# Kernel tuning notes

Measured on AMD Instinct MI355X. Metric: run time of the kernel, lower is better.

## Reference

```python
import jax, jax.numpy as jnp
import numpy as np

EMBED_DIM = 512
NUM_HEADS = 8
HEAD_DIM = EMBED_DIM // NUM_HEADS
K_NEIGH = 3
SEQ_N = 16384
BATCH = 4


def setup_inputs() -> dict:
    key = jax.random.key(0)
    ks = jax.random.split(key, 12)
    x = jax.random.normal(ks[0], (BATCH, SEQ_N, EMBED_DIM), dtype=jnp.float32)
    neighbor_table = jax.random.randint(ks[1], (K_NEIGH, SEQ_N), 0, SEQ_N, dtype=jnp.int64)
    s = 0.02
    Wq = jax.random.normal(ks[2], (EMBED_DIM, EMBED_DIM), jnp.float32) * s
    bq = jnp.zeros((EMBED_DIM,), jnp.float32)
    Wk = jax.random.normal(ks[3], (EMBED_DIM, EMBED_DIM), jnp.float32) * s
    bk = jnp.zeros((EMBED_DIM,), jnp.float32)
    Wv = jax.random.normal(ks[4], (EMBED_DIM, EMBED_DIM), jnp.float32) * s
    bv = jnp.zeros((EMBED_DIM,), jnp.float32)
    Wo = jax.random.normal(ks[5], (EMBED_DIM, EMBED_DIM), jnp.float32) * s
    bo = jnp.zeros((EMBED_DIM,), jnp.float32)
    return {"x": x, "neighbor_table": neighbor_table,
            "Wq": Wq, "bq": bq, "Wk": Wk, "bk": bk,
            "Wv": Wv, "bv": bv, "Wo": Wo, "bo": bo}


def reference(x, neighbor_table, Wq, bq, Wk, bk, Wv, bv, Wo, bo):
    B, N, C = x.shape
    H, d = NUM_HEADS, HEAD_DIM
    scale = d ** (-0.5)
    # buffers derived from neighbor_table (matches module __init__)
    valid = (neighbor_table != -1)                      # (K, N)
    idx = jnp.clip(neighbor_table, 0)                   # (K, N)

    # projections; nn.Linear: y = x @ W.T + b
    def proj(W, b):
        return (jnp.einsum('bnc,oc->bno', x, W) + b).reshape(B, N, H, d).transpose(0, 2, 1, 3)  # (B,H,N,d)

    q = proj(Wq, bq)
    k = proj(Wk, bk)
    v = proj(Wv, bv)

    # gather neighbors: (B, H, K, N, d)
    k_nb = k[:, :, idx, :]
    v_nb = v[:, :, idx, :]

    # scores over head_dim: (B, H, K, N)
    scores = jnp.einsum('bhnd,bhknd->bhkn', q, k_nb) * scale
    scores = jnp.where(valid[None, None], scores, -jnp.inf)
    attn = jax.nn.softmax(scores, axis=2)               # softmax over K neighbors
    # dropout is identity (eval / p used only at train)

    out = jnp.einsum('bhkn,bhknd->bhnd', attn, v_nb)    # (B,H,N,d)
    out = out.transpose(0, 2, 1, 3).reshape(B, N, C)
    out = jnp.einsum('bnc,oc->bno', out, Wo) + bo
    return out
```

## Files before the change

### kernel.cpp

```cpp
#include <hip/hip_runtime.h>
#include <stdint.h>

#define SEQN 16384
#define NBATCH 4

typedef __attribute__((ext_vector_type(8))) __bf16 bf16x8;
typedef __attribute__((ext_vector_type(4))) float f32x4;
typedef __attribute__((ext_vector_type(4))) unsigned int u32x4;

__device__ __forceinline__ unsigned int f2bf(float f) {
  unsigned int x = __builtin_bit_cast(unsigned int, f);
  x = x + 0x7fffu + ((x >> 16) & 1u);
  return x >> 16;
}
__device__ __forceinline__ float bf2f(unsigned int lo) {
  return __builtin_bit_cast(float, lo << 16);
}

__device__ __forceinline__ void gload_lds16(const unsigned short* g, unsigned char* l) {
  __builtin_amdgcn_global_load_lds(
      (const __attribute__((address_space(1))) unsigned int*)g,
      (__attribute__((address_space(3))) unsigned int*)l, 16, 0, 0);
}

template<bool OUT_BF16>
__global__ __launch_bounds__(256, 2)
void gemm_bt(const unsigned short* __restrict__ A,
             const unsigned short* __restrict__ Bt,
             const float* __restrict__ bias,
             void* __restrict__ Cout,
             int Ncols, int K)
{
  __shared__ __align__(16) unsigned char lA[128 * 64 * 2];
  __shared__ __align__(16) unsigned char lB[128 * 64 * 2];
  const int tid = threadIdx.x;
  const int lane = tid & 63;
  const int wid = tid >> 6;
  const int wr = (wid >> 1) * 64;
  const int wc = (wid & 1) * 64;
  const int nbx = Ncols >> 7;
  const int bx = (int)blockIdx.x % nbx;
  const int by = (int)blockIdx.x / nbx;
  const long row0 = (long)by << 7;
  const int col0 = bx << 7;

  f32x4 acc[4][4];
#pragma unroll
  for (int i = 0; i < 4; ++i)
#pragma unroll
    for (int j = 0; j < 4; ++j) acc[i][j] = (f32x4)0.0f;

  for (int kt = 0; kt < K; kt += 64) {
#pragma unroll
    for (int i = 0; i < 4; ++i) {
      const int f = i * 256 + tid;
      const int r = f >> 3;
      const int cd = (f & 7) ^ (r & 7);
      gload_lds16(A + (row0 + r) * (long)K + kt + cd * 8, lA + f * 16);
      gload_lds16(Bt + (long)(col0 + r) * K + kt + cd * 8, lB + f * 16);
    }
    __syncthreads();
#pragma unroll
    for (int kk = 0; kk < 2; ++kk) {
      bf16x8 af[4], bfv[4];
#pragma unroll
      for (int fm = 0; fm < 4; ++fm) {
        const int row = wr + fm * 16 + (lane & 15);
        const int ch = (kk * 4 + (lane >> 4)) ^ (row & 7);
        af[fm] = __builtin_bit_cast(bf16x8, *(const u32x4*)(lA + row * 128 + ch * 16));
      }
#pragma unroll
      for (int fn = 0; fn < 4; ++fn) {
        const int row = wc + fn * 16 + (lane & 15);
        const int ch = (kk * 4 + (lane >> 4)) ^ (row & 7);
        bfv[fn] = __builtin_bit_cast(bf16x8, *(const u32x4*)(lB + row * 128 + ch * 16));
      }
#pragma unroll
      for (int fm = 0; fm < 4; ++fm)
#pragma unroll
        for (int fn = 0; fn < 4; ++fn)
          acc[fm][fn] = __builtin_amdgcn_mfma_f32_16x16x32_bf16(af[fm], bfv[fn], acc[fm][fn], 0, 0, 0);
    }
    __syncthreads();
  }

#pragma unroll
  for (int fn = 0; fn < 4; ++fn) {
    const int n = col0 + wc + fn * 16 + (lane & 15);
    const float bn = bias[n];
#pragma unroll
    for (int fm = 0; fm < 4; ++fm) {
      const long mbase = row0 + wr + fm * 16 + ((lane >> 4) << 2);
#pragma unroll
      for (int j = 0; j < 4; ++j) {
        const float v = acc[fm][fn][j] + bn;
        if constexpr (OUT_BF16)
          ((unsigned short*)Cout)[(mbase + j) * (long)Ncols + n] = (unsigned short)f2bf(v);
        else
          ((float*)Cout)[(mbase + j) * (long)Ncols + n] = v;
      }
    }
  }
}

__global__ __launch_bounds__(256)
void nbr_attn(const unsigned short* __restrict__ qkv,
              const int* __restrict__ nbr,
              unsigned short* __restrict__ aout)
{
  const int wid = (int)((blockIdx.x * 256 + threadIdx.x) >> 6);
  const int lane = threadIdx.x & 63;
  const int n = wid & (SEQN - 1);
  const int b = wid >> 14;

  const unsigned short* qrow = qkv + (size_t)wid * 1536;
  float qv[8];
  {
    const u32x4 raw = *(const u32x4*)(qrow + lane * 8);
#pragma unroll
    for (int i = 0; i < 4; ++i) {
      qv[2 * i] = bf2f(raw[i] & 0xffffu);
      qv[2 * i + 1] = bf2f(raw[i] >> 16);
    }
  }
  float s[3];
  u32x4 vraw[3];
  bool val[3];
#pragma unroll
  for (int k = 0; k < 3; ++k) {
    const int t = nbr[k * SEQN + n];
    val[k] = (t != -1);
    const int j = t > 0 ? t : 0;
    const unsigned short* krow = qkv + ((size_t)(b * SEQN + j)) * 1536 + 512;
    const u32x4 kraw = *(const u32x4*)(krow + lane * 8);
    vraw[k] = *(const u32x4*)(krow + 512 + lane * 8);
    float d = 0.f;
#pragma unroll
    for (int i = 0; i < 4; ++i)
      d += qv[2 * i] * bf2f(kraw[i] & 0xffffu) + qv[2 * i + 1] * bf2f(kraw[i] >> 16);
    d += __shfl_xor(d, 1);
    d += __shfl_xor(d, 2);
    d += __shfl_xor(d, 4);
    s[k] = d * 0.125f;
  }
  float m = -3.0e38f;
#pragma unroll
  for (int k = 0; k < 3; ++k)
    if (val[k]) m = fmaxf(m, s[k]);
  float e[3], sum = 0.f;
#pragma unroll
  for (int k = 0; k < 3; ++k) {
    e[k] = val[k] ? __expf(s[k] - m) : 0.f;
    sum += e[k];
  }
  const float inv = sum > 0.f ? 1.f / sum : 0.f;
  float acc[8] = {0.f, 0.f, 0.f, 0.f, 0.f, 0.f, 0.f, 0.f};
#pragma unroll
  for (int k = 0; k < 3; ++k) {
    const float w = e[k] * inv;
#pragma unroll
    for (int i = 0; i < 4; ++i) {
      acc[2 * i] += w * bf2f(vraw[k][i] & 0xffffu);
      acc[2 * i + 1] += w * bf2f(vraw[k][i] >> 16);
    }
  }
  u32x4 o;
#pragma unroll
  for (int i = 0; i < 4; ++i)
    o[i] = f2bf(acc[2 * i]) | (f2bf(acc[2 * i + 1]) << 16);
  *(u32x4*)(aout + (size_t)wid * 512 + lane * 8) = o;
}

__global__ __launch_bounds__(256)
void cvt_f32_bf16(const float* __restrict__ in, unsigned short* __restrict__ out, int n8) {
  int i = blockIdx.x * 256 + threadIdx.x;
  const int stride = gridDim.x * 256;
  for (; i < n8; i += stride) {
    const float4* p = (const float4*)(in + (size_t)i * 8);
    const float4 a = p[0], c = p[1];
    u32x4 o;
    o[0] = f2bf(a.x) | (f2bf(a.y) << 16);
    o[1] = f2bf(a.z) | (f2bf(a.w) << 16);
    o[2] = f2bf(c.x) | (f2bf(c.y) << 16);
    o[3] = f2bf(c.z) | (f2bf(c.w) << 16);
    *(u32x4*)(out + (size_t)i * 8) = o;
  }
}

__global__ __launch_bounds__(256)
void prep_w(const float* __restrict__ Wq, const float* __restrict__ Wk,
            const float* __restrict__ Wv, const float* __restrict__ Wo,
            const float* __restrict__ bq, const float* __restrict__ bk,
            const float* __restrict__ bv,
            unsigned short* __restrict__ wf, unsigned short* __restrict__ wo,
            float* __restrict__ biasf)
{
  const int i = blockIdx.x * 256 + threadIdx.x;
  const int stride = gridDim.x * 256;
  for (int t = i; t < 262144; t += stride) {
    wf[t] = (unsigned short)f2bf(Wq[t]);
    wf[262144 + t] = (unsigned short)f2bf(Wk[t]);
    wf[524288 + t] = (unsigned short)f2bf(Wv[t]);
    wo[t] = (unsigned short)f2bf(Wo[t]);
  }
  if (i < 512) {
    biasf[i] = bq[i];
    biasf[512 + i] = bk[i];
    biasf[1024 + i] = bv[i];
  }
}

extern "C" void kernel_launch(void* const* d_in, const int* in_sizes, int n_in,
                              void* d_out, int out_size, void* d_ws, size_t ws_size,
                              hipStream_t stream) {
  const float* x  = (const float*)d_in[0];
  const int* nbr  = (const int*)d_in[1];
  const float* Wq = (const float*)d_in[2];
  const float* bq = (const float*)d_in[3];
  const float* Wk = (const float*)d_in[4];
  const float* bk = (const float*)d_in[5];
  const float* Wv = (const float*)d_in[6];
  const float* bv = (const float*)d_in[7];
  const float* Wo = (const float*)d_in[8];
  const float* bo = (const float*)d_in[9];
  float* out = (float*)d_out;
  unsigned char* ws = (unsigned char*)d_ws;

  unsigned short* xb  = (unsigned short*)(ws);
  unsigned short* qkv = (unsigned short*)(ws + 67108864UL);
  unsigned short* wf  = (unsigned short*)(ws + 268435456UL);
  unsigned short* wo  = (unsigned short*)(ws + 270008320UL);
  float* biasf        = (float*)(ws + 270532608UL);

  cvt_f32_bf16<<<4096, 256, 0, stream>>>(x, xb, 33554432 / 8);
  prep_w<<<1024, 256, 0, stream>>>(Wq, Wk, Wv, Wo, bq, bk, bv, wf, wo, biasf);
  gemm_bt<true><<<dim3(512 * 12), 256, 0, stream>>>(xb, wf, biasf, qkv, 1536, 512);
  nbr_attn<<<16384, 256, 0, stream>>>(qkv, nbr, xb);
  gemm_bt<false><<<dim3(512 * 4), 256, 0, stream>>>(xb, wo, bo, out, 512, 512);
}
```

Baseline: 298.5 us.

## Rewrite GEMM as 256x256-tile, 4-stage pipelined kernel with XCD-aware block swizzle

Replaces the 128x128 single-buffered GEMM with a 512-thread 256x256-tile kernel that keeps four K-slices of 32 in flight in 128 KB of dynamic LDS, using explicit vmcnt waits so global-to-LDS loads overlap the MFMA work. Block IDs are remapped across the eight XCDs to improve L2 reuse, and MFMA sections raise wave priority. The larger tile reduces global traffic per FLOP, at the cost of one block per CU, a hard-coded K=512, and fewer blocks for the output projection (512 blocks).

```diff
diff --git a/kernel.cpp b/kernel.cpp
--- a/kernel.cpp
+++ b/kernel.cpp
@@ -24,72 +24,112 @@
 }
 
 template<bool OUT_BF16>
-__global__ __launch_bounds__(256, 2)
-void gemm_bt(const unsigned short* __restrict__ A,
+__global__ __launch_bounds__(512, 1)
+void gemm256(const unsigned short* __restrict__ A,
              const unsigned short* __restrict__ Bt,
              const float* __restrict__ bias,
              void* __restrict__ Cout,
-             int Ncols, int K)
+             int Ncols)
 {
-  __shared__ __align__(16) unsigned char lA[128 * 64 * 2];
-  __shared__ __align__(16) unsigned char lB[128 * 64 * 2];
+  extern __shared__ __align__(16) unsigned char smem[];
+  const int K = 512;
   const int tid = threadIdx.x;
   const int lane = tid & 63;
   const int wid = tid >> 6;
-  const int wr = (wid >> 1) * 64;
-  const int wc = (wid & 1) * 64;
-  const int nbx = Ncols >> 7;
-  const int bx = (int)blockIdx.x % nbx;
-  const int by = (int)blockIdx.x / nbx;
-  const long row0 = (long)by << 7;
-  const int col0 = bx << 7;
-
-  f32x4 acc[4][4];
-#pragma unroll
-  for (int i = 0; i < 4; ++i)
+  const int wr = (wid >> 2) << 7;
+  const int wc = (wid & 3) << 6;
+  const int nbx = Ncols >> 8;
+  const int nwg = (int)gridDim.x;
+  const int bid = (int)blockIdx.x;
+  const int cpx = nwg >> 3;
+  const int swz = (bid & 7) * cpx + (bid >> 3);
+  const int bx = swz % nbx;
+  const int by = swz / nbx;
+  const long row0 = (long)by << 8;
+  const int col0 = bx << 8;
+
+  int srcA[2], srcB[2];
+#pragma unroll
+  for (int i = 0; i < 2; ++i) {
+    const int G = i * 512 + tid;
+    const int r = G >> 2;
+    const int c = (G & 3) ^ ((G >> 3) & 3);
+    srcA[i] = (int)(row0 + r) * K + c * 8;
+    srcB[i] = (col0 + r) * K + c * 8;
+  }
+
+  int aoff[8], boff[4];
+#pragma unroll
+  for (int fm = 0; fm < 8; ++fm) {
+    const int r = wr + fm * 16 + (lane & 15);
+    aoff[fm] = r * 64 + ((((lane >> 4)) ^ ((r >> 1) & 3)) << 4);
+  }
+#pragma unroll
+  for (int fn = 0; fn < 4; ++fn) {
+    const int r = wc + fn * 16 + (lane & 15);
+    boff[fn] = r * 64 + ((((lane >> 4)) ^ ((r >> 1) & 3)) << 4);
+  }
+
+  f32x4 acc[8][4];
+#pragma unroll
+  for (int i = 0; i < 8; ++i)
 #pragma unroll
     for (int j = 0; j < 4; ++j) acc[i][j] = (f32x4)0.0f;
 
-  for (int kt = 0; kt < K; kt += 64) {
-#pragma unroll
-    for (int i = 0; i < 4; ++i) {
-      const int f = i * 256 + tid;
-      const int r = f >> 3;
-      const int cd = (f & 7) ^ (r & 7);
-      gload_lds16(A + (row0 + r) * (long)K + kt + cd * 8, lA + f * 16);
-      gload_lds16(Bt + (long)(col0 + r) * K + kt + cd * 8, lB + f * 16);
-    }
+#define STAGE(t)                                                            \
+  {                                                                         \
+    unsigned char* buf_ = smem + ((t) & 3) * 32768;                         \
+    const int kt_ = (t) * 32;                                               \
+    gload_lds16(A + srcA[0] + kt_, buf_ + tid * 16);                        \
+    gload_lds16(Bt + srcB[0] + kt_, buf_ + 16384 + tid * 16);               \
+    gload_lds16(A + srcA[1] + kt_, buf_ + 8192 + tid * 16);                 \
+    gload_lds16(Bt + srcB[1] + kt_, buf_ + 24576 + tid * 16);               \
+  }
+
+#define COMPUTE(t)                                                          \
+  {                                                                         \
+    const unsigned char* buf_ = smem + ((t) & 3) * 32768;                   \
+    bf16x8 af[8], bfv[4];                                                   \
+    _Pragma("unroll")                                                       \
+    for (int fm = 0; fm < 8; ++fm)                                          \
+      af[fm] = __builtin_bit_cast(bf16x8, *(const u32x4*)(buf_ + aoff[fm]));\
+    _Pragma("unroll")                                                       \
+    for (int fn = 0; fn < 4; ++fn)                                          \
+      bfv[fn] = __builtin_bit_cast(bf16x8,                                  \
+                    *(const u32x4*)(buf_ + 16384 + boff[fn]));              \
+    __builtin_amdgcn_s_setprio(1);                                          \
+    _Pragma("unroll")                                                       \
+    for (int fm = 0; fm < 8; ++fm)                                          \
+      _Pragma("unroll")                                                     \
+      for (int fn = 0; fn < 4; ++fn)                                        \
+        acc[fm][fn] = __builtin_amdgcn_mfma_f32_16x16x32_bf16(              \
+            af[fm], bfv[fn], acc[fm][fn], 0, 0, 0);                         \
+    __builtin_amdgcn_s_setprio(0);                                          \
+  }
+
+  STAGE(0); STAGE(1); STAGE(2);
+  for (int t = 0; t < 13; ++t) {
+    STAGE(t + 3);
+    asm volatile("s_waitcnt vmcnt(12)" ::: "memory");
     __syncthreads();
-#pragma unroll
-    for (int kk = 0; kk < 2; ++kk) {
-      bf16x8 af[4], bfv[4];
-#pragma unroll
-      for (int fm = 0; fm < 4; ++fm) {
-        const int row = wr + fm * 16 + (lane & 15);
-        const int ch = (kk * 4 + (lane >> 4)) ^ (row & 7);
-        af[fm] = __builtin_bit_cast(bf16x8, *(const u32x4*)(lA + row * 128 + ch * 16));
-      }
-#pragma unroll
-      for (int fn = 0; fn < 4; ++fn) {
-        const int row = wc + fn * 16 + (lane & 15);
-        const int ch = (kk * 4 + (lane >> 4)) ^ (row & 7);
-        bfv[fn] = __builtin_bit_cast(bf16x8, *(const u32x4*)(lB + row * 128 + ch * 16));
-      }
-#pragma unroll
-      for (int fm = 0; fm < 4; ++fm)
-#pragma unroll
-        for (int fn = 0; fn < 4; ++fn)
-          acc[fm][fn] = __builtin_amdgcn_mfma_f32_16x16x32_bf16(af[fm], bfv[fn], acc[fm][fn], 0, 0, 0);
-    }
+    COMPUTE(t);
     __syncthreads();
   }
+  asm volatile("s_waitcnt vmcnt(8)" ::: "memory");
+  __syncthreads(); COMPUTE(13); __syncthreads();
+  asm volatile("s_waitcnt vmcnt(4)" ::: "memory");
+  __syncthreads(); COMPUTE(14); __syncthreads();
+  asm volatile("s_waitcnt vmcnt(0)" ::: "memory");
+  __syncthreads(); COMPUTE(15);
+#undef STAGE
+#undef COMPUTE
 
 #pragma unroll
   for (int fn = 0; fn < 4; ++fn) {
     const int n = col0 + wc + fn * 16 + (lane & 15);
     const float bn = bias[n];
 #pragma unroll
-    for (int fm = 0; fm < 4; ++fm) {
+    for (int fm = 0; fm < 8; ++fm) {
       const long mbase = row0 + wr + fm * 16 + ((lane >> 4) << 2);
 #pragma unroll
       for (int j = 0; j < 4; ++j) {
@@ -232,9 +272,18 @@
   unsigned short* wo  = (unsigned short*)(ws + 270008320UL);
   float* biasf        = (float*)(ws + 270532608UL);
 
+  static bool attr_done = false;
+  if (!attr_done) {
+    hipFuncSetAttribute((const void*)gemm256<true>,
+                        hipFuncAttributeMaxDynamicSharedMemorySize, 131072);
+    hipFuncSetAttribute((const void*)gemm256<false>,
+                        hipFuncAttributeMaxDynamicSharedMemorySize, 131072);
+    attr_done = true;
+  }
+
   cvt_f32_bf16<<<4096, 256, 0, stream>>>(x, xb, 33554432 / 8);
   prep_w<<<1024, 256, 0, stream>>>(Wq, Wk, Wv, Wo, bq, bk, bv, wf, wo, biasf);
-  gemm_bt<true><<<dim3(512 * 12), 256, 0, stream>>>(xb, wf, biasf, qkv, 1536, 512);
+  gemm256<true><<<dim3(256 * 6), 512, 131072, stream>>>(xb, wf, biasf, qkv, 1536);
   nbr_attn<<<16384, 256, 0, stream>>>(qkv, nbr, xb);
-  gemm_bt<false><<<dim3(512 * 4), 256, 0, stream>>>(xb, wo, bo, out, 512, 512);
-}
+  gemm256<false><<<dim3(256 * 2), 512, 131072, stream>>>(xb, wo, bo, out, 512);
+}
```

Result: slower. 375.1 us (+25.7%).
